# Performance work log

Hardware: AMD Instinct MI355X
Metric: run time of the kernel (lower is better)

Reference implementation:

```python
import jax, jax.numpy as jnp
import numpy as np

IN_FEATS, H_FEATS, OUT_FEATS = 128, 256, 64
N_NODES, N_EDGES = 50000, 800000
DROP_P = 0.5


def setup_inputs() -> dict:
    key = jax.random.key(0)
    k_h, k_e, k_w1, k_w2 = jax.random.split(key, 4)
    h = jax.random.normal(k_h, (N_NODES, IN_FEATS), dtype=jnp.float32)
    edge_index = jax.random.randint(k_e, (2, N_EDGES), 0, N_NODES, dtype=jnp.int64)
    # Glorot-style init for GraphConv weights; bias zeros (DGL default)
    W1 = jax.random.normal(k_w1, (IN_FEATS, H_FEATS), dtype=jnp.float32) / np.sqrt(IN_FEATS)
    b1 = jnp.zeros((H_FEATS,), dtype=jnp.float32)
    W2 = jax.random.normal(k_w2, (H_FEATS, OUT_FEATS), dtype=jnp.float32) / np.sqrt(H_FEATS)
    b2 = jnp.zeros((OUT_FEATS,), dtype=jnp.float32)
    return {"h": h, "W1": W1, "b1": b1, "W2": W2, "b2": b2,
            "edge_index": edge_index, "n_nodes": N_NODES}


def _sym_norm(edge_index, n_nodes):
    # symmetric GCN norm: deg^-1/2 on both endpoints (in-degree, clamped to 1)
    dst = edge_index[1]
    deg = jax.ops.segment_sum(jnp.ones(edge_index.shape[1], jnp.float32), dst,
                              num_segments=n_nodes)
    return jnp.where(deg > 0, deg, 1.0) ** -0.5  # [N]


def _graph_conv(h, W, b, src, dst, norm, n_nodes, apply_w_first):
    # DGL GraphConv (norm='both'): scale by src norm, aggregate, scale by dst norm.
    # W is applied before aggregation if in_feats > out_feats, else after.
    x = h * norm[:, None]
    if apply_w_first:
        x = x @ W
    agg = jax.ops.segment_sum(x[src], dst, num_segments=n_nodes)
    if not apply_w_first:
        agg = agg @ W
    return agg * norm[:, None] + b


def reference(h, W1, b1, W2, b2, edge_index, n_nodes):
    src, dst = edge_index[0], edge_index[1]
    norm = _sym_norm(edge_index, n_nodes)
    # layer 1: in(128) <= out(256) -> aggregate then transform; relu activation
    h1 = jax.nn.relu(_graph_conv(h, W1, b1, src, dst, norm, n_nodes, apply_w_first=False))
    # dropout(0.5), training mode, deterministic key
    keep = jax.random.bernoulli(jax.random.key(42), 1.0 - DROP_P, h1.shape)
    h1 = jnp.where(keep, h1 / (1.0 - DROP_P), 0.0)
    # layer 2: in(256) > out(64) -> transform then aggregate; no activation
    out = _graph_conv(h1, W2, b2, src, dst, norm, n_nodes, apply_w_first=True)
    return out
```

## Files before the change

### kernel.cpp

```cpp
#include <hip/hip_runtime.h>
#include <stdint.h>

#define N_IN  128
#define N_H   256
#define N_OUT 64
#define CHK   2048
#define CAP   6144

typedef __attribute__((ext_vector_type(8))) __bf16 bf16x8;
typedef __attribute__((ext_vector_type(4))) float f32x4;

__device__ __forceinline__ void tf4(uint32_t& x0, uint32_t& x1,
                                    const int r0, const int r1, const int r2, const int r3) {
  x0 += x1; x1 = (x1 << r0) | (x1 >> (32 - r0)); x1 ^= x0;
  x0 += x1; x1 = (x1 << r1) | (x1 >> (32 - r1)); x1 ^= x0;
  x0 += x1; x1 = (x1 << r2) | (x1 >> (32 - r2)); x1 ^= x0;
  x0 += x1; x1 = (x1 << r3) | (x1 >> (32 - r3)); x1 ^= x0;
}

__device__ __forceinline__ uint2 threefry2x32(uint32_t k0, uint32_t k1, uint32_t x0, uint32_t x1) {
  const uint32_t k2 = k0 ^ k1 ^ 0x1BD11BDAu;
  x0 += k0; x1 += k1;
  tf4(x0, x1, 13, 15, 26, 6);   x0 += k1; x1 += k2 + 1u;
  tf4(x0, x1, 17, 29, 16, 24);  x0 += k2; x1 += k0 + 2u;
  tf4(x0, x1, 13, 15, 26, 6);   x0 += k0; x1 += k1 + 3u;
  tf4(x0, x1, 17, 29, 16, 24);  x0 += k1; x1 += k2 + 4u;
  tf4(x0, x1, 13, 15, 26, 6);   x0 += k2; x1 += k0 + 5u;
  return make_uint2(x0, x1);
}

__device__ __forceinline__ uint16_t f2bf_rne(float v) {
  uint32_t b = __builtin_bit_cast(uint32_t, v);
  b += 0x7fffu + ((b >> 16) & 1u);
  return (uint16_t)(b >> 16);
}
__device__ __forceinline__ float bflo(uint32_t w) { return __builtin_bit_cast(float, w << 16); }
__device__ __forceinline__ float bfhi(uint32_t w) { return __builtin_bit_cast(float, w & 0xffff0000u); }

__device__ __forceinline__ void packW_body(const float* __restrict__ W,
                                           uint4* __restrict__ WH, uint4* __restrict__ WL,
                                           int Ncols, int nct, int nks, int g) {
  if (g >= nct * nks * 64) return;
  int lane = g & 63;
  int grp = g >> 6;
  int ks = grp % nks, ct = grp / nks;
  int k0 = ks * 32 + (lane >> 4) * 8;
  int col = ct * 16 + (lane & 15);
  uint32_t hb[8], lb[8];
#pragma unroll
  for (int j = 0; j < 8; j++) {
    float w = W[(size_t)(k0 + j) * Ncols + col];
    uint32_t bits = __builtin_bit_cast(uint32_t, w);
    uint32_t hi = bits & 0xffff0000u;
    float lo = w - __builtin_bit_cast(float, hi);
    hb[j] = hi >> 16;
    lb[j] = __builtin_bit_cast(uint32_t, lo) >> 16;
  }
  WH[g] = make_uint4(hb[0] | (hb[1] << 16), hb[2] | (hb[3] << 16),
                     hb[4] | (hb[5] << 16), hb[6] | (hb[7] << 16));
  WL[g] = make_uint4(lb[0] | (lb[1] << 16), lb[2] | (lb[3] << 16),
                     lb[4] | (lb[5] << 16), lb[6] | (lb[7] << 16));
}

__global__ __launch_bounds__(256) void k_front(
    const int* __restrict__ eidx, int E, int* __restrict__ bktCur, uint2* __restrict__ eb,
    uint16_t* __restrict__ mask, int N,
    const float* __restrict__ W1, uint4* __restrict__ W1H, uint4* __restrict__ W1L,
    const float* __restrict__ W2, uint4* __restrict__ W2H, uint4* __restrict__ W2L,
    int NBE) {
  const int b = blockIdx.x, t = threadIdx.x;
  if (b < NBE) {
    __shared__ int s_nz;
    __shared__ int hist[256];
    __shared__ int base[256];
    if (t == 0) s_nz = 0;
    hist[t] = 0;
    __syncthreads();
    int n = E < 2048 ? E : 2048;
    int nz = 0;
    for (int i = t; i < n; i += 256) nz |= (eidx[2 * i + 1] != 0) ? 1 : 0;
    if (nz) atomicAdd(&s_nz, 1);
    __syncthreads();
    int stride = (s_nz == 0) ? 2 : 1;

    int cb = b * CHK;
    int dc[8], sc[8];
#pragma unroll
    for (int i = 0; i < 8; i++) {
      int e = cb + i * 256 + t;
      if (e < E) {
        dc[i] = eidx[(size_t)(E + e) * stride];
        sc[i] = eidx[(size_t)e * stride];
        atomicAdd(&hist[dc[i] >> 8], 1);
      } else dc[i] = -1;
    }
    __syncthreads();
    int hcnt = hist[t];
    if (hcnt) base[t] = atomicAdd(&bktCur[t], hcnt);
    __syncthreads();
    hist[t] = 0;
    __syncthreads();
#pragma unroll
    for (int i = 0; i < 8; i++) {
      if (dc[i] >= 0) {
        int bk = dc[i] >> 8;
        int r = atomicAdd(&hist[bk], 1);
        eb[(size_t)bk * CAP + base[bk] + r] = make_uint2((unsigned)sc[i], (unsigned)dc[i]);
      }
    }
  } else {
    const int NBM = (N * 16 + 255) >> 8;
    int bb = b - NBE;
    if (bb < NBM) {
      int g = bb * 256 + t;
      if (g >= N * 16) return;
      uint32_t row = (uint32_t)(g >> 4), colb = (uint32_t)(g & 15);
      uint32_t bse = row * 256u + colb;
      uint32_t m = 0;
#pragma unroll
      for (int ct = 0; ct < 16; ct++) {
        uint2 o = threefry2x32(0u, 42u, 0u, bse + (uint32_t)ct * 16u);
        uint32_t bits = o.x ^ o.y;
        m |= ((~bits) >> 31) << ct;
      }
      mask[g] = (uint16_t)m;
    } else if (bb < NBM + 16) {
      packW_body(W1, W1H, W1L, N_H, 16, 4, (bb - NBM) * 256 + t);
    } else {
      packW_body(W2, W2H, W2L, N_OUT, 4, 8, (bb - NBM - 16) * 256 + t);
    }
  }
}

__global__ __launch_bounds__(256) void k_bucket_csr(
    const uint2* __restrict__ eb, const int* __restrict__ bktCur,
    int* __restrict__ rowptr, float* __restrict__ norm,
    int* __restrict__ esrc, int N, int E) {
  __shared__ int s[256];
  __shared__ int cnt[256];
  __shared__ int pfx[256];
  __shared__ int cur[256];
  const int b = blockIdx.x, t = threadIdx.x;
  if (b == 0 && t == 0) rowptr[N] = E;
  if (b * 256 >= N) return;
  int xc = bktCur[t];
  s[t] = xc;
  __syncthreads();
  for (int off = 1; off < 256; off <<= 1) {
    int u = (t >= off) ? s[t - off] : 0;
    __syncthreads();
    s[t] += u;
    __syncthreads();
  }
  const int lo = (b > 0) ? s[b - 1] : 0;
  const int ecnt = s[b] - lo;
  const uint2* ebb = eb + (size_t)b * CAP;
  cnt[t] = 0;
  __syncthreads();
  for (int e = t; e < ecnt; e += 256)
    atomicAdd(&cnt[ebb[e].y & 255u], 1);
  __syncthreads();
  int x = cnt[t];
  pfx[t] = x;
  __syncthreads();
  for (int off = 1; off < 256; off <<= 1) {
    int u = (t >= off) ? pfx[t - off] : 0;
    __syncthreads();
    pfx[t] += u;
    __syncthreads();
  }
  int excl = pfx[t] - x;
  int node = b * 256 + t;
  if (node < N) {
    rowptr[node] = lo + excl;
    norm[node] = x > 0 ? rsqrtf((float)x) : 1.0f;
  }
  cur[t] = excl;
  __syncthreads();
  for (int e = t; e < ecnt; e += 256) {
    uint2 r = ebb[e];
    int d = (int)(r.y & 255u);
    int p = atomicAdd(&cur[d], 1);
    esrc[lo + p] = (int)r.x;
  }
}

__global__ __launch_bounds__(256) void k_mid(
    int* __restrict__ esrc, const int* __restrict__ rowptr, int N,
    const float* __restrict__ h, const float* __restrict__ norm,
    uint16_t* __restrict__ hn, int NS) {
  const int b = blockIdx.x, t = threadIdx.x;
  if (b < NS) {
    int node = b * 4 + (t >> 6);
    if (node >= N) return;
    const int lane = t & 63;
    int lo = rowptr[node], hi = rowptr[node + 1], d = hi - lo;
    if (d <= 1) return;
    if (d <= 64) {
      int v = (lane < d) ? esrc[lo + lane] : 0x7fffffff;
#pragma unroll
      for (int k = 2; k <= 64; k <<= 1) {
#pragma unroll
        for (int j = k >> 1; j > 0; j >>= 1) {
          int other = __shfl_xor(v, j);
          bool up = ((lane & k) == 0);
          bool lower = ((lane & j) == 0);
          int mn = min(v, other), mx = max(v, other);
          v = (up == lower) ? mn : mx;
        }
      }
      if (lane < d) esrc[lo + lane] = v;
    } else if (lane == 0) {
      for (int i = lo + 1; i < hi; i++) {
        int v = esrc[i];
        int j = i - 1;
        while (j >= lo && esrc[j] > v) { esrc[j + 1] = esrc[j]; j--; }
        esrc[j + 1] = v;
      }
    }
  } else {
    int g = (b - NS) * 256 + t;
    if (g >= N * 32) return;
    float nr = norm[g >> 5];
    float4 v = *reinterpret_cast<const float4*>(h + (size_t)g * 4);
    ushort4 r;
    r.x = f2bf_rne(v.x * nr);
    r.y = f2bf_rne(v.y * nr);
    r.z = f2bf_rne(v.z * nr);
    r.w = f2bf_rne(v.w * nr);
    *reinterpret_cast<ushort4*>(hn + (size_t)g * 4) = r;
  }
}

__global__ __launch_bounds__(256) void k_pull1(
    const uint16_t* __restrict__ hn, const int* __restrict__ rowptr,
    const int* __restrict__ esrc, uint16_t* __restrict__ aggB, int N) {
  int node = blockIdx.x * 8 + (threadIdx.x >> 5);
  if (node >= N) return;
  int lane = threadIdx.x & 31;
  int lo = rowptr[node], hi = rowptr[node + 1];
  float4 a0 = {0,0,0,0}, a1 = {0,0,0,0}, a2 = {0,0,0,0}, a3 = {0,0,0,0};
  int e = lo;
  for (; e + 7 < hi; e += 8) {
    int s0 = esrc[e],     s1 = esrc[e + 1], s2 = esrc[e + 2], s3 = esrc[e + 3];
    int s4 = esrc[e + 4], s5 = esrc[e + 5], s6 = esrc[e + 6], s7 = esrc[e + 7];
    uint2 v0 = *reinterpret_cast<const uint2*>(hn + (size_t)s0 * N_IN + lane * 4);
    uint2 v1 = *reinterpret_cast<const uint2*>(hn + (size_t)s1 * N_IN + lane * 4);
    uint2 v2 = *reinterpret_cast<const uint2*>(hn + (size_t)s2 * N_IN + lane * 4);
    uint2 v3 = *reinterpret_cast<const uint2*>(hn + (size_t)s3 * N_IN + lane * 4);
    uint2 v4 = *reinterpret_cast<const uint2*>(hn + (size_t)s4 * N_IN + lane * 4);
    uint2 v5 = *reinterpret_cast<const uint2*>(hn + (size_t)s5 * N_IN + lane * 4);
    uint2 v6 = *reinterpret_cast<const uint2*>(hn + (size_t)s6 * N_IN + lane * 4);
    uint2 v7 = *reinterpret_cast<const uint2*>(hn + (size_t)s7 * N_IN + lane * 4);
    a0.x += bflo(v0.x); a0.y += bfhi(v0.x); a0.z += bflo(v0.y); a0.w += bfhi(v0.y);
    a1.x += bflo(v1.x); a1.y += bfhi(v1.x); a1.z += bflo(v1.y); a1.w += bfhi(v1.y);
    a2.x += bflo(v2.x); a2.y += bfhi(v2.x); a2.z += bflo(v2.y); a2.w += bfhi(v2.y);
    a3.x += bflo(v3.x); a3.y += bfhi(v3.x); a3.z += bflo(v3.y); a3.w += bfhi(v3.y);
    a0.x += bflo(v4.x); a0.y += bfhi(v4.x); a0.z += bflo(v4.y); a0.w += bfhi(v4.y);
    a1.x += bflo(v5.x); a1.y += bfhi(v5.x); a1.z += bflo(v5.y); a1.w += bfhi(v5.y);
    a2.x += bflo(v6.x); a2.y += bfhi(v6.x); a2.z += bflo(v6.y); a2.w += bfhi(v6.y);
    a3.x += bflo(v7.x); a3.y += bfhi(v7.x); a3.z += bflo(v7.y); a3.w += bfhi(v7.y);
  }
  for (; e < hi; e++) {
    uint2 v0 = *reinterpret_cast<const uint2*>(hn + (size_t)esrc[e] * N_IN + lane * 4);
    a0.x += bflo(v0.x); a0.y += bfhi(v0.x); a0.z += bflo(v0.y); a0.w += bfhi(v0.y);
  }
  float4 r;
  r.x = (a0.x + a1.x) + (a2.x + a3.x);
  r.y = (a0.y + a1.y) + (a2.y + a3.y);
  r.z = (a0.z + a1.z) + (a2.z + a3.z);
  r.w = (a0.w + a1.w) + (a2.w + a3.w);
  ushort4 p = make_ushort4(f2bf_rne(r.x), f2bf_rne(r.y), f2bf_rne(r.z), f2bf_rne(r.w));
  *reinterpret_cast<ushort4*>(aggB + (size_t)node * N_IN + lane * 4) = p;
}

__global__ __launch_bounds__(256) void k_gemm1_mfma(
    const uint16_t* __restrict__ aggB, const uint4* __restrict__ WH,
    const uint4* __restrict__ WL, const float* __restrict__ b1,
    const float* __restrict__ norm, const uint16_t* __restrict__ mask,
    uint16_t* __restrict__ h1sB, int Nn) {
  const int tid = threadIdx.x;
  const int wave = tid >> 6, lane = tid & 63;
  const int row0 = blockIdx.x * 64 + wave * 16;
  const int cy = blockIdx.y;
  const int lrow = lane & 15, lk = lane >> 4;
  int arow = row0 + lrow; if (arow >= Nn) arow = Nn - 1;

  f32x4 acc[8];
#pragma unroll
  for (int c = 0; c < 8; c++) acc[c] = f32x4{0.f, 0.f, 0.f, 0.f};

#pragma unroll
  for (int ks = 0; ks < 4; ks++) {
    union { uint4 q; bf16x8 v; } ah;
    ah.q = *reinterpret_cast<const uint4*>(aggB + (size_t)arow * N_IN + ks * 32 + lk * 8);
#pragma unroll
    for (int c = 0; c < 8; c++) {
      int ct = cy * 8 + c;
      union { uint4 q; bf16x8 v; } bh, bl;
      bh.q = WH[(ct * 4 + ks) * 64 + lane];
      bl.q = WL[(ct * 4 + ks) * 64 + lane];
      acc[c] = __builtin_amdgcn_mfma_f32_16x16x32_bf16(ah.v, bh.v, acc[c], 0, 0, 0);
      acc[c] = __builtin_amdgcn_mfma_f32_16x16x32_bf16(ah.v, bl.v, acc[c], 0, 0, 0);
    }
  }

  const int colb = lane & 15, rgrp = lane >> 4;
#pragma unroll
  for (int r = 0; r < 4; r++) {
    int row = row0 + rgrp * 4 + r;
    if (row >= Nn) continue;
    float nr = norm[row];
    uint32_t m = mask[row * 16 + colb];
#pragma unroll
    for (int c = 0; c < 8; c++) {
      int ct = cy * 8 + c;
      int col = ct * 16 + colb;
      float v = fmaf(acc[c][r], nr, b1[col]);
      v = fmaxf(v, 0.f);
      v = ((m >> ct) & 1u) ? v * (2.0f * nr) : 0.f;
      h1sB[(size_t)row * N_H + col] = f2bf_rne(v);
    }
  }
}

__global__ __launch_bounds__(256) void k_gemm2_mfma(
    const uint16_t* __restrict__ h1sB, const uint4* __restrict__ WH,
    const uint4* __restrict__ WL, uint16_t* __restrict__ zbf, int Nn) {
  const int tid = threadIdx.x;
  const int wave = tid >> 6, lane = tid & 63;
  const int row0 = blockIdx.x * 64 + wave * 16;
  const int lrow = lane & 15, lk = lane >> 4;
  int arow = row0 + lrow; if (arow >= Nn) arow = Nn - 1;

  f32x4 acc[4];
#pragma unroll
  for (int ct = 0; ct < 4; ct++) acc[ct] = f32x4{0.f, 0.f, 0.f, 0.f};

#pragma unroll
  for (int ks = 0; ks < 8; ks++) {
    union { uint4 q; bf16x8 v; } ah;
    ah.q = *reinterpret_cast<const uint4*>(h1sB + (size_t)arow * N_H + ks * 32 + lk * 8);
#pragma unroll
    for (int ct = 0; ct < 4; ct++) {
      union { uint4 q; bf16x8 v; } bh, bl;
      bh.q = WH[(ct * 8 + ks) * 64 + lane];
      bl.q = WL[(ct * 8 + ks) * 64 + lane];
      acc[ct] = __builtin_amdgcn_mfma_f32_16x16x32_bf16(ah.v, bh.v, acc[ct], 0, 0, 0);
      acc[ct] = __builtin_amdgcn_mfma_f32_16x16x32_bf16(ah.v, bl.v, acc[ct], 0, 0, 0);
    }
  }

  const int colb = lane & 15, rgrp = lane >> 4;
#pragma unroll
  for (int r = 0; r < 4; r++) {
    int row = row0 + rgrp * 4 + r;
    if (row >= Nn) continue;
#pragma unroll
    for (int ct = 0; ct < 4; ct++)
      zbf[(size_t)row * N_OUT + ct * 16 + colb] = f2bf_rne(acc[ct][r]);
  }
}

__global__ __launch_bounds__(256) void k_pull2(
    const uint16_t* __restrict__ zbf, const float* __restrict__ norm,
    const float* __restrict__ b2, const int* __restrict__ rowptr,
    const int* __restrict__ esrc, float* __restrict__ out, int N) {
  int node = blockIdx.x * 16 + (threadIdx.x >> 4);
  if (node >= N) return;
  int lane = threadIdx.x & 15;
  int lo = rowptr[node], hi = rowptr[node + 1];
  float4 a0 = {0,0,0,0}, a1 = {0,0,0,0}, a2 = {0,0,0,0}, a3 = {0,0,0,0};
  int e = lo;
  for (; e + 7 < hi; e += 8) {
    int s0 = esrc[e],     s1 = esrc[e + 1], s2 = esrc[e + 2], s3 = esrc[e + 3];
    int s4 = esrc[e + 4], s5 = esrc[e + 5], s6 = esrc[e + 6], s7 = esrc[e + 7];
    uint2 v0 = *reinterpret_cast<const uint2*>(zbf + (size_t)s0 * N_OUT + lane * 4);
    uint2 v1 = *reinterpret_cast<const uint2*>(zbf + (size_t)s1 * N_OUT + lane * 4);
    uint2 v2 = *reinterpret_cast<const uint2*>(zbf + (size_t)s2 * N_OUT + lane * 4);
    uint2 v3 = *reinterpret_cast<const uint2*>(zbf + (size_t)s3 * N_OUT + lane * 4);
    uint2 v4 = *reinterpret_cast<const uint2*>(zbf + (size_t)s4 * N_OUT + lane * 4);
    uint2 v5 = *reinterpret_cast<const uint2*>(zbf + (size_t)s5 * N_OUT + lane * 4);
    uint2 v6 = *reinterpret_cast<const uint2*>(zbf + (size_t)s6 * N_OUT + lane * 4);
    uint2 v7 = *reinterpret_cast<const uint2*>(zbf + (size_t)s7 * N_OUT + lane * 4);
    a0.x += bflo(v0.x); a0.y += bfhi(v0.x); a0.z += bflo(v0.y); a0.w += bfhi(v0.y);
    a1.x += bflo(v1.x); a1.y += bfhi(v1.x); a1.z += bflo(v1.y); a1.w += bfhi(v1.y);
    a2.x += bflo(v2.x); a2.y += bfhi(v2.x); a2.z += bflo(v2.y); a2.w += bfhi(v2.y);
    a3.x += bflo(v3.x); a3.y += bfhi(v3.x); a3.z += bflo(v3.y); a3.w += bfhi(v3.y);
    a0.x += bflo(v4.x); a0.y += bfhi(v4.x); a0.z += bflo(v4.y); a0.w += bfhi(v4.y);
    a1.x += bflo(v5.x); a1.y += bfhi(v5.x); a1.z += bflo(v5.y); a1.w += bfhi(v5.y);
    a2.x += bflo(v6.x); a2.y += bfhi(v6.x); a2.z += bflo(v6.y); a2.w += bfhi(v6.y);
    a3.x += bflo(v7.x); a3.y += bfhi(v7.x); a3.z += bflo(v7.y); a3.w += bfhi(v7.y);
  }
  for (; e < hi; e++) {
    uint2 v0 = *reinterpret_cast<const uint2*>(zbf + (size_t)esrc[e] * N_OUT + lane * 4);
    a0.x += bflo(v0.x); a0.y += bfhi(v0.x); a0.z += bflo(v0.y); a0.w += bfhi(v0.y);
  }
  float nn = norm[node];
  float4 bb = *reinterpret_cast<const float4*>(b2 + lane * 4);
  float4 r;
  r.x = ((a0.x + a1.x) + (a2.x + a3.x)) * nn + bb.x;
  r.y = ((a0.y + a1.y) + (a2.y + a3.y)) * nn + bb.y;
  r.z = ((a0.z + a1.z) + (a2.z + a3.z)) * nn + bb.z;
  r.w = ((a0.w + a1.w) + (a2.w + a3.w)) * nn + bb.w;
  *reinterpret_cast<float4*>(out + (size_t)node * N_OUT + lane * 4) = r;
}

extern "C" void kernel_launch(void* const* d_in, const int* in_sizes, int n_in,
                              void* d_out, int out_size, void* d_ws, size_t ws_size,
                              hipStream_t stream) {
  const float* h  = (const float*)d_in[0];
  const float* W1 = (const float*)d_in[1];
  const float* b1 = (const float*)d_in[2];
  const float* W2 = (const float*)d_in[3];
  const float* b2 = (const float*)d_in[4];
  const int* eidx = (const int*)d_in[5];
  const int N = in_sizes[0] / N_IN;
  const int E = in_sizes[5] / 2;
  const int NBE = (E + CHK - 1) / CHK;
  const int NBM = (N * 16 + 255) / 256;
  const int NS  = (N + 3) / 4;
  const int NH  = (N * 32 + 255) / 256;

  char* ws = (char*)d_ws;
  size_t off = 0;
  auto alloc = [&](size_t bytes) { void* p = ws + off; off += (bytes + 511) & ~(size_t)511; return p; };
  int*      rowptr = (int*)alloc((size_t)(N + 1) * 4);
  float*    norm   = (float*)alloc((size_t)N * 4);
  int*      esrc   = (int*)alloc((size_t)E * 4);
  int*      bktCur = (int*)alloc((size_t)256 * 4);
  uint16_t* mask   = (uint16_t*)alloc((size_t)N * 16 * 2);
  uint4*    W1H    = (uint4*)alloc((size_t)16 * 4 * 64 * 16);
  uint4*    W1L    = (uint4*)alloc((size_t)16 * 4 * 64 * 16);
  uint4*    W2H    = (uint4*)alloc((size_t)4 * 8 * 64 * 16);
  uint4*    W2L    = (uint4*)alloc((size_t)4 * 8 * 64 * 16);
  uint2*    eb     = (uint2*)alloc((size_t)256 * CAP * 8);
  uint16_t* aggB   = (uint16_t*)alloc((size_t)N * N_IN * 2);
  uint16_t* h1sB   = (uint16_t*)alloc((size_t)N * N_H * 2);
  uint16_t* hn     = (uint16_t*)h1sB;
  uint16_t* zbf    = (uint16_t*)aggB;
  float*    out    = (float*)d_out;

  hipMemsetAsync(bktCur, 0, 256 * 4, stream);

  k_front<<<NBE + NBM + 16 + 8, 256, 0, stream>>>(eidx, E, bktCur, eb,
                                                  mask, N, W1, W1H, W1L, W2, W2H, W2L, NBE);

  k_bucket_csr<<<256, 256, 0, stream>>>(eb, bktCur, rowptr, norm, esrc, N, E);

  k_mid<<<NS + NH, 256, 0, stream>>>(esrc, rowptr, N, h, norm, hn, NS);

  k_pull1<<<(N + 7) / 8, 256, 0, stream>>>(hn, rowptr, esrc, aggB, N);

  dim3 g1((N + 63) / 64, 2);
  k_gemm1_mfma<<<g1, 256, 0, stream>>>(aggB, W1H, W1L, b1, norm, mask, h1sB, N);
  k_gemm2_mfma<<<(N + 63) / 64, 256, 0, stream>>>(h1sB, W2H, W2L, zbf, N);

  k_pull2<<<(N + 15) / 16, 256, 0, stream>>>(zbf, norm, b2, rowptr, esrc, out, N);
}
```

Before: 163.5 us.

## Fuse both GEMMs into one kernel keeping hidden activations in LDS

```diff
diff --git a/kernel.cpp b/kernel.cpp
--- a/kernel.cpp
+++ b/kernel.cpp
@@ -274,91 +274,82 @@
   *reinterpret_cast<ushort4*>(aggB + (size_t)node * N_IN + lane * 4) = p;
 }
 
-__global__ __launch_bounds__(256) void k_gemm1_mfma(
-    const uint16_t* __restrict__ aggB, const uint4* __restrict__ WH,
-    const uint4* __restrict__ WL, const float* __restrict__ b1,
-    const float* __restrict__ norm, const uint16_t* __restrict__ mask,
-    uint16_t* __restrict__ h1sB, int Nn) {
-  const int tid = threadIdx.x;
-  const int wave = tid >> 6, lane = tid & 63;
-  const int row0 = blockIdx.x * 64 + wave * 16;
-  const int cy = blockIdx.y;
-  const int lrow = lane & 15, lk = lane >> 4;
-  int arow = row0 + lrow; if (arow >= Nn) arow = Nn - 1;
-
-  f32x4 acc[8];
-#pragma unroll
-  for (int c = 0; c < 8; c++) acc[c] = f32x4{0.f, 0.f, 0.f, 0.f};
-
-#pragma unroll
-  for (int ks = 0; ks < 4; ks++) {
-    union { uint4 q; bf16x8 v; } ah;
-    ah.q = *reinterpret_cast<const uint4*>(aggB + (size_t)arow * N_IN + ks * 32 + lk * 8);
-#pragma unroll
-    for (int c = 0; c < 8; c++) {
-      int ct = cy * 8 + c;
-      union { uint4 q; bf16x8 v; } bh, bl;
-      bh.q = WH[(ct * 4 + ks) * 64 + lane];
-      bl.q = WL[(ct * 4 + ks) * 64 + lane];
-      acc[c] = __builtin_amdgcn_mfma_f32_16x16x32_bf16(ah.v, bh.v, acc[c], 0, 0, 0);
-      acc[c] = __builtin_amdgcn_mfma_f32_16x16x32_bf16(ah.v, bl.v, acc[c], 0, 0, 0);
-    }
-  }
-
-  const int colb = lane & 15, rgrp = lane >> 4;
-#pragma unroll
-  for (int r = 0; r < 4; r++) {
-    int row = row0 + rgrp * 4 + r;
-    if (row >= Nn) continue;
-    float nr = norm[row];
-    uint32_t m = mask[row * 16 + colb];
-#pragma unroll
-    for (int c = 0; c < 8; c++) {
-      int ct = cy * 8 + c;
-      int col = ct * 16 + colb;
-      float v = fmaf(acc[c][r], nr, b1[col]);
-      v = fmaxf(v, 0.f);
-      v = ((m >> ct) & 1u) ? v * (2.0f * nr) : 0.f;
-      h1sB[(size_t)row * N_H + col] = f2bf_rne(v);
-    }
-  }
-}
-
-__global__ __launch_bounds__(256) void k_gemm2_mfma(
-    const uint16_t* __restrict__ h1sB, const uint4* __restrict__ WH,
-    const uint4* __restrict__ WL, uint16_t* __restrict__ zbf, int Nn) {
+__global__ __launch_bounds__(256) void k_gemm12(
+    const uint16_t* __restrict__ aggB,
+    const uint4* __restrict__ W1H, const uint4* __restrict__ W1L,
+    const float* __restrict__ b1, const float* __restrict__ norm,
+    const uint16_t* __restrict__ mask,
+    const uint4* __restrict__ W2H, const uint4* __restrict__ W2L,
+    uint16_t* __restrict__ zbf, int Nn) {
+  __shared__ uint16_t h1[64 * 256];
   const int tid = threadIdx.x;
   const int wave = tid >> 6, lane = tid & 63;
   const int row0 = blockIdx.x * 64 + wave * 16;
   const int lrow = lane & 15, lk = lane >> 4;
   int arow = row0 + lrow; if (arow >= Nn) arow = Nn - 1;
 
-  f32x4 acc[4];
-#pragma unroll
-  for (int ct = 0; ct < 4; ct++) acc[ct] = f32x4{0.f, 0.f, 0.f, 0.f};
-
+  f32x4 acc[16];
+#pragma unroll
+  for (int c = 0; c < 16; c++) acc[c] = f32x4{0.f, 0.f, 0.f, 0.f};
+#pragma unroll
+  for (int ks = 0; ks < 4; ks++) {
+    union { uint4 q; bf16x8 v; } ah;
+    ah.q = *reinterpret_cast<const uint4*>(aggB + (size_t)arow * N_IN + ks * 32 + lk * 8);
+#pragma unroll
+    for (int c = 0; c < 16; c++) {
+      union { uint4 q; bf16x8 v; } bh, bl;
+      bh.q = W1H[(c * 4 + ks) * 64 + lane];
+      bl.q = W1L[(c * 4 + ks) * 64 + lane];
+      acc[c] = __builtin_amdgcn_mfma_f32_16x16x32_bf16(ah.v, bh.v, acc[c], 0, 0, 0);
+      acc[c] = __builtin_amdgcn_mfma_f32_16x16x32_bf16(ah.v, bl.v, acc[c], 0, 0, 0);
+    }
+  }
+
+  const int colb = lane & 15, rgrp = lane >> 4;
+#pragma unroll
+  for (int r = 0; r < 4; r++) {
+    int lrw = wave * 16 + rgrp * 4 + r;
+    int row = blockIdx.x * 64 + lrw;
+    float nr = (row < Nn) ? norm[row] : 0.f;
+    uint32_t m = (row < Nn) ? (uint32_t)mask[row * 16 + colb] : 0u;
+    int sw = (lrw & 7) << 3;
+#pragma unroll
+    for (int c = 0; c < 16; c++) {
+      int col = c * 16 + colb;
+      float v = fmaf(acc[c][r], nr, b1[col]);
+      v = fmaxf(v, 0.f);
+      v = ((m >> c) & 1u) ? v * (2.0f * nr) : 0.f;
+      h1[lrw * 256 + (col ^ sw)] = f2bf_rne(v);
+    }
+  }
+  __syncthreads();
+
+  f32x4 acc2[4];
+#pragma unroll
+  for (int c = 0; c < 4; c++) acc2[c] = f32x4{0.f, 0.f, 0.f, 0.f};
+  const int myrow = wave * 16 + lrow;
+  const int sw2 = (myrow & 7) << 3;
 #pragma unroll
   for (int ks = 0; ks < 8; ks++) {
     union { uint4 q; bf16x8 v; } ah;
-    ah.q = *reinterpret_cast<const uint4*>(h1sB + (size_t)arow * N_H + ks * 32 + lk * 8);
-#pragma unroll
-    for (int ct = 0; ct < 4; ct++) {
+    int c0 = (ks * 32 + lk * 8) ^ sw2;
+    ah.q = *reinterpret_cast<const uint4*>(&h1[myrow * 256 + c0]);
+#pragma unroll
+    for (int c = 0; c < 4; c++) {
       union { uint4 q; bf16x8 v; } bh, bl;
-      bh.q = WH[(ct * 8 + ks) * 64 + lane];
-      bl.q = WL[(ct * 8 + ks) * 64 + lane];
-      acc[ct] = __builtin_amdgcn_mfma_f32_16x16x32_bf16(ah.v, bh.v, acc[ct], 0, 0, 0);
-      acc[ct] = __builtin_amdgcn_mfma_f32_16x16x32_bf16(ah.v, bl.v, acc[ct], 0, 0, 0);
-    }
-  }
-
-  const int colb = lane & 15, rgrp = lane >> 4;
+      bh.q = W2H[(c * 8 + ks) * 64 + lane];
+      bl.q = W2L[(c * 8 + ks) * 64 + lane];
+      acc2[c] = __builtin_amdgcn_mfma_f32_16x16x32_bf16(ah.v, bh.v, acc2[c], 0, 0, 0);
+      acc2[c] = __builtin_amdgcn_mfma_f32_16x16x32_bf16(ah.v, bl.v, acc2[c], 0, 0, 0);
+    }
+  }
 #pragma unroll
   for (int r = 0; r < 4; r++) {
     int row = row0 + rgrp * 4 + r;
     if (row >= Nn) continue;
 #pragma unroll
-    for (int ct = 0; ct < 4; ct++)
-      zbf[(size_t)row * N_OUT + ct * 16 + colb] = f2bf_rne(acc[ct][r]);
+    for (int c = 0; c < 4; c++)
+      zbf[(size_t)row * N_OUT + c * 16 + colb] = f2bf_rne(acc2[c][r]);
   }
 }
 
@@ -435,10 +426,9 @@
   uint4*    W2H    = (uint4*)alloc((size_t)4 * 8 * 64 * 16);
   uint4*    W2L    = (uint4*)alloc((size_t)4 * 8 * 64 * 16);
   uint2*    eb     = (uint2*)alloc((size_t)256 * CAP * 8);
+  uint16_t* hn     = (uint16_t*)alloc((size_t)N * N_IN * 2);
   uint16_t* aggB   = (uint16_t*)alloc((size_t)N * N_IN * 2);
-  uint16_t* h1sB   = (uint16_t*)alloc((size_t)N * N_H * 2);
-  uint16_t* hn     = (uint16_t*)h1sB;
-  uint16_t* zbf    = (uint16_t*)aggB;
+  uint16_t* zbf    = (uint16_t*)alloc((size_t)N * N_OUT * 2);
   float*    out    = (float*)d_out;
 
   hipMemsetAsync(bktCur, 0, 256 * 4, stream);
@@ -452,9 +442,8 @@
 
   k_pull1<<<(N + 7) / 8, 256, 0, stream>>>(hn, rowptr, esrc, aggB, N);
 
-  dim3 g1((N + 63) / 64, 2);
-  k_gemm1_mfma<<<g1, 256, 0, stream>>>(aggB, W1H, W1L, b1, norm, mask, h1sB, N);
-  k_gemm2_mfma<<<(N + 63) / 64, 256, 0, stream>>>(h1sB, W2H, W2L, zbf, N);
+  k_gemm12<<<(N + 63) / 64, 256, 0, stream>>>(aggB, W1H, W1L, b1, norm, mask,
+                                              W2H, W2L, zbf, N);
 
   k_pull2<<<(N + 15) / 16, 256, 0, stream>>>(zbf, norm, b2, rowptr, esrc, out, N);
 }
```

Result: no change. 164.6 us (+0.6%).
